# Kernel tuning notes

Hardware: AMD Instinct MI355X
Metric: run time of the kernel (lower is better)

Reference implementation:

```python
import jax, jax.numpy as jnp
import numpy as np

DIM = 768
NUM_HEADS = 12
SCALE = 1.0 / (DIM ** 0.5)  # NOTE: source scales by 1/sqrt(dim), not 1/sqrt(head_dim)


def setup_inputs() -> dict:
    key = jax.random.key(0)
    k_x, k_qkv, k_ow, k_ob = jax.random.split(key, 4)
    b, n = 8, 1024
    x = jax.random.normal(k_x, (b, n, DIM), dtype=jnp.float32)
    # torch Linear weight is [out, in]; we store jax-style [in, out]
    w_qkv = jax.random.normal(k_qkv, (DIM, 3 * DIM), dtype=jnp.float32) * (DIM ** -0.5)
    w_out = jax.random.normal(k_ow, (DIM, DIM), dtype=jnp.float32) * (DIM ** -0.5)
    b_out = jax.random.normal(k_ob, (DIM,), dtype=jnp.float32) * 0.01
    return {"x": x, "w_qkv": w_qkv, "w_out": w_out, "b_out": b_out}


def reference(x, w_qkv, w_out, b_out):
    b, n, c = x.shape
    h = NUM_HEADS
    hd = c // h
    qkv = (x @ w_qkv).reshape(b, n, 3, h, hd)
    q, k, v = jnp.moveaxis(qkv, 2, 0)          # each [b, n, h, hd]
    q = jnp.swapaxes(q, 1, 2)                  # [b, h, n, hd]
    k = jnp.swapaxes(k, 1, 2)
    v = jnp.swapaxes(v, 1, 2)
    dot = jnp.einsum('bhqd,bhkd->bhqk', q, k) * SCALE
    attn = jax.nn.softmax(dot, axis=-1)        # attn_dropout p=0 -> identity
    out = jnp.einsum('bhqk,bhkd->bhqd', attn, v)
    out = jnp.swapaxes(out, 1, 2).reshape(b, n, c)
    return out @ w_out + b_out                 # proj_dropout p=0 -> identity
```

## Files before the change

kernel.cpp:

```cpp
#include <hip/hip_runtime.h>

#define DEV __device__ __forceinline__

typedef __bf16 bf16x8 __attribute__((ext_vector_type(8)));
typedef float  f32x4  __attribute__((ext_vector_type(4)));
typedef float  f32x16 __attribute__((ext_vector_type(16)));
typedef unsigned int u32x4 __attribute__((ext_vector_type(4)));

static constexpr float SCALE = 0.036084391824351615f;
static constexpr float L2E   = 1.4426950408889634f;

DEV unsigned short f2bf(float f) {
  return __builtin_bit_cast(unsigned short, (__bf16)f);
}
DEV unsigned int pack2(float a, float b) {
  return (unsigned int)f2bf(a) | ((unsigned int)f2bf(b) << 16);
}

#define GLDS16(gp, lp) \
  __builtin_amdgcn_global_load_lds((__attribute__((address_space(1))) void*)(gp), \
                                   (__attribute__((address_space(3))) void*)(lp), 16, 0, 0)

__global__ __launch_bounds__(256) void k_prep(const float* __restrict__ x,
                                              const float* __restrict__ w_qkv,
                                              const float* __restrict__ w_out,
                                              unsigned short* __restrict__ xb,
                                              unsigned short* __restrict__ wqkvT,
                                              unsigned short* __restrict__ woutT) {
  __shared__ float tile[64][65];
  int b = blockIdx.x, t = threadIdx.x;
  if (b < 3072) {
    int i = b * 256 + t;
    const float4* p = (const float4*)x + (size_t)i * 2;
    float4 a = p[0], bb = p[1];
    uint4 r;
    r.x = pack2(a.x, a.y); r.y = pack2(a.z, a.w);
    r.z = pack2(bb.x, bb.y); r.w = pack2(bb.z, bb.w);
    ((uint4*)xb)[i] = r;
    return;
  }
  const float* in;
  unsigned short* out;
  int R, C, bx, by;
  if (b < 3504) {
    int tt = b - 3072; in = w_qkv; out = wqkvT; R = 768; C = 2304;
    bx = tt % 36; by = tt / 36;
  } else {
    int tt = b - 3504; in = w_out; out = woutT; R = 768; C = 768;
    bx = tt % 12; by = tt / 12;
  }
  int c0 = bx * 64, r0 = by * 64;
  int tr = t >> 6, tc = t & 63;
#pragma unroll
  for (int i = 0; i < 64; i += 4)
    tile[i + tr][tc] = in[(size_t)(r0 + i + tr) * C + c0 + tc];
  __syncthreads();
#pragma unroll
  for (int i = 0; i < 64; i += 4)
    out[(size_t)(c0 + i + tr) * R + r0 + tc] = f2bf(tile[tc][i + tr]);
}

__global__ __launch_bounds__(512, 4) void k_gemm1(const unsigned short* __restrict__ A,
                                                  const unsigned short* __restrict__ BT,
                                                  unsigned short* __restrict__ Qb,
                                                  unsigned short* __restrict__ Kb,
                                                  unsigned short* __restrict__ VTb) {
  __shared__ __align__(16) char smem[49152];
  char* As = smem;
  char* Bs = smem + 16384;
  const int tid = threadIdx.x;
  const int wave = tid >> 6, lane = tid & 63;
  const int g = lane >> 4, l15 = lane & 15;
  const int wrow = wave >> 2, wcol = wave & 3;

  int id = blockIdx.y * gridDim.x + blockIdx.x;
  int per_xcd = (gridDim.x * gridDim.y) >> 3;
  int id2 = (id & 7) * per_xcd + (id >> 3);
  const int bm = id2 / gridDim.x, bn = id2 % gridDim.x;

  f32x4 acc[4][4] = {};
  const unsigned short* Abase = A + (size_t)bm * 128 * 768;
  const unsigned short* Bbase = BT + (size_t)bn * 256 * 768;

  for (int kt = 0; kt < 12; ++kt) {
    const int k0 = kt * 64;
#pragma unroll
    for (int i = 0; i < 2; ++i) {
      int q = i * 512 + tid;
      int row = q >> 3, c = q & 7;
      int cs = c ^ (row & 7);
      GLDS16(Abase + (size_t)row * 768 + k0 + cs * 8, As + (i * 512 + wave * 64) * 16);
    }
#pragma unroll
    for (int i = 0; i < 4; ++i) {
      int q = i * 512 + tid;
      int row = q >> 3, c = q & 7;
      int cs = c ^ (row & 7);
      GLDS16(Bbase + (size_t)row * 768 + k0 + cs * 8, Bs + (i * 512 + wave * 64) * 16);
    }
    __syncthreads();
    __builtin_amdgcn_s_setprio(1);
#pragma unroll
    for (int kk = 0; kk < 2; ++kk) {
      bf16x8 af[4], bfr[4];
#pragma unroll
      for (int mi = 0; mi < 4; ++mi) {
        int r = wrow * 64 + mi * 16 + l15;
        af[mi] = *(const bf16x8*)(As + r * 128 + (((kk * 4 + g) ^ (r & 7)) * 16));
      }
#pragma unroll
      for (int ni = 0; ni < 4; ++ni) {
        int r = wcol * 64 + ni * 16 + l15;
        bfr[ni] = *(const bf16x8*)(Bs + r * 128 + (((kk * 4 + g) ^ (r & 7)) * 16));
      }
#pragma unroll
      for (int mi = 0; mi < 4; ++mi)
#pragma unroll
        for (int ni = 0; ni < 4; ++ni)
          acc[mi][ni] = __builtin_amdgcn_mfma_f32_16x16x32_bf16(af[mi], bfr[ni], acc[mi][ni], 0, 0, 0);
    }
    __builtin_amdgcn_s_setprio(0);
    __syncthreads();
  }

  const int row0 = bm * 128 + wrow * 64;
  const int col0 = bn * 256 + wcol * 64;
#pragma unroll
  for (int mi = 0; mi < 4; ++mi) {
#pragma unroll
    for (int ni = 0; ni < 4; ++ni) {
      int col = col0 + ni * 16 + l15;
      int which = col / 768;
      int hd = col - which * 768;
      int head = hd >> 6, d = hd & 63;
      int rowm0 = row0 + mi * 16 + g * 4;
      int bi = rowm0 >> 10, np = rowm0 & 1023;
      if (which == 0) {
#pragma unroll
        for (int j = 0; j < 4; ++j)
          Qb[((size_t)(bi * 12 + head) * 1024 + np + j) * 64 + d] =
              f2bf(acc[mi][ni][j] * (SCALE * L2E));
      } else if (which == 1) {
#pragma unroll
        for (int j = 0; j < 4; ++j)
          Kb[((size_t)(bi * 12 + head) * 1024 + np + j) * 64 + d] = f2bf(acc[mi][ni][j]);
      } else {
        ushort4 w;
        w.x = f2bf(acc[mi][ni][0]); w.y = f2bf(acc[mi][ni][1]);
        w.z = f2bf(acc[mi][ni][2]); w.w = f2bf(acc[mi][ni][3]);
        *(ushort4*)(VTb + ((size_t)(bi * 12 + head) * 64 + d) * 1024 + np) = w;
      }
    }
  }
}

__global__ __launch_bounds__(256) void k_gemm2(const unsigned short* __restrict__ A,
                                               const unsigned short* __restrict__ BT,
                                               float* __restrict__ out,
                                               const float* __restrict__ bias) {
  __shared__ __align__(16) char smem[65536];
  const int tid = threadIdx.x;
  const int wave = tid >> 6, lane = tid & 63;
  const int g = lane >> 4, l15 = lane & 15;
  const int wrow = wave >> 1, wcol = wave & 1;

  int id = blockIdx.y * gridDim.x + blockIdx.x;
  int per_xcd = (gridDim.x * gridDim.y) >> 3;
  int id2 = (id & 7) * per_xcd + (id >> 3);
  const int bm = id2 / gridDim.x, bn = id2 % gridDim.x;

  f32x4 acc[4][4] = {};
  const unsigned short* Abase = A + (size_t)bm * 128 * 768;
  const unsigned short* Bbase = BT + (size_t)bn * 128 * 768;

  auto STAGE = [&](int buf, int kt) {
    const int k0 = kt * 64;
#pragma unroll
    for (int i = 0; i < 4; ++i) {
      int q = i * 256 + tid;
      int row = q >> 3, c = q & 7;
      int cs = c ^ (row & 7);
      GLDS16(Abase + (size_t)row * 768 + k0 + cs * 8,
             smem + buf * 32768 + (i * 256 + wave * 64) * 16);
      GLDS16(Bbase + (size_t)row * 768 + k0 + cs * 8,
             smem + buf * 32768 + 16384 + (i * 256 + wave * 64) * 16);
    }
  };

  STAGE(0, 0);
  __syncthreads();

#pragma unroll
  for (int kt = 0; kt < 12; ++kt) {
    const int cur = kt & 1;
    if (kt < 11) STAGE(cur ^ 1, kt + 1);
    char* As = smem + cur * 32768;
    char* Bs = As + 16384;
    __builtin_amdgcn_s_setprio(1);
#pragma unroll
    for (int kk = 0; kk < 2; ++kk) {
      bf16x8 af[4], bfr[4];
#pragma unroll
      for (int mi = 0; mi < 4; ++mi) {
        int r = wrow * 64 + mi * 16 + l15;
        af[mi] = *(const bf16x8*)(As + r * 128 + (((kk * 4 + g) ^ (r & 7)) * 16));
      }
#pragma unroll
      for (int ni = 0; ni < 4; ++ni) {
        int r = wcol * 64 + ni * 16 + l15;
        bfr[ni] = *(const bf16x8*)(Bs + r * 128 + (((kk * 4 + g) ^ (r & 7)) * 16));
      }
#pragma unroll
      for (int mi = 0; mi < 4; ++mi)
#pragma unroll
        for (int ni = 0; ni < 4; ++ni)
          acc[mi][ni] = __builtin_amdgcn_mfma_f32_16x16x32_bf16(af[mi], bfr[ni], acc[mi][ni], 0, 0, 0);
    }
    __builtin_amdgcn_s_setprio(0);
    __syncthreads();
  }

  const int row0 = bm * 128 + wrow * 64;
  const int col0 = bn * 128 + wcol * 64;
#pragma unroll
  for (int mi = 0; mi < 4; ++mi) {
#pragma unroll
    for (int ni = 0; ni < 4; ++ni) {
      int col = col0 + ni * 16 + l15;
      float bz = bias[col];
#pragma unroll
      for (int j = 0; j < 4; ++j) {
        int rowm = row0 + mi * 16 + g * 4 + j;
        out[(size_t)rowm * 768 + col] = acc[mi][ni][j] + bz;
      }
    }
  }
}

__global__ __launch_bounds__(256, 3) void k_attn(const unsigned short* __restrict__ Qb,
                                                 const unsigned short* __restrict__ Kb,
                                                 const unsigned short* __restrict__ VTb,
                                                 unsigned short* __restrict__ Ao) {
  __shared__ __align__(16) char smem[32768];
  const int tid = threadIdx.x, wave = tid >> 6, lane = tid & 63;
  const int hi = lane >> 5, q31 = lane & 31;
  const int bh = blockIdx.x % 96, qt = blockIdx.x / 96;
  const int qbase = qt * 128 + wave * 32;
  const unsigned short* Kp = Kb + (size_t)bh * 65536;
  const unsigned short* Vp = VTb + (size_t)bh * 65536;

  auto STAGE = [&](int buf, int kt) {
#pragma unroll
    for (int i = 0; i < 2; ++i) {
      int c = i * 4 + wave;
      GLDS16(Kp + (size_t)(kt * 64 + lane) * 64 + c * 8,
             smem + buf * 8192 + (i * 256 + wave * 64) * 16);
      GLDS16(Vp + (size_t)lane * 1024 + kt * 64 + c * 8,
             smem + 16384 + buf * 8192 + (i * 256 + wave * 64) * 16);
    }
  };

  bf16x8 aq[4];
#pragma unroll
  for (int dk = 0; dk < 4; ++dk)
    aq[dk] = *(const bf16x8*)(Qb + (size_t)bh * 65536 +
                              (size_t)(qbase + q31) * 64 + dk * 16 + hi * 8);

  bf16x8 vones;
#pragma unroll
  for (int e = 0; e < 8; ++e) vones[e] = (__bf16)1.0f;

  f32x16 o0 = {}, o1 = {};
  f32x16 lacc = {};

  STAGE(0, 0);
  __syncthreads();

#pragma unroll 2
  for (int kt = 0; kt < 16; ++kt) {
    const int cur = kt & 1;
    if (kt < 15) STAGE(cur ^ 1, kt + 1);
    char* Ks = smem + cur * 8192;
    char* Vs = smem + 16384 + cur * 8192;

    f32x16 st0 = {}, st1 = {};
    __builtin_amdgcn_s_setprio(1);
#pragma unroll
    for (int dk = 0; dk < 4; ++dk) {
      bf16x8 ka0 = *(const bf16x8*)(Ks + (((dk * 2 + hi) * 64 + q31) * 16));
      bf16x8 ka1 = *(const bf16x8*)(Ks + (((dk * 2 + hi) * 64 + 32 + q31) * 16));
      st0 = __builtin_amdgcn_mfma_f32_32x32x16_bf16(ka0, aq[dk], st0, 0, 0, 0);
      st1 = __builtin_amdgcn_mfma_f32_32x32x16_bf16(ka1, aq[dk], st1, 0, 0, 0);
    }
    __builtin_amdgcn_s_setprio(0);

#pragma unroll
    for (int sub = 0; sub < 2; ++sub) {
      const f32x16& st = sub ? st1 : st0;
      float ex[16];
#pragma unroll
      for (int r2 = 0; r2 < 16; ++r2) ex[r2] = __builtin_amdgcn_exp2f(st[r2]);

      unsigned w00 = pack2(ex[0], ex[1]),   w01 = pack2(ex[2], ex[3]);
      unsigned w10 = pack2(ex[4], ex[5]),   w11 = pack2(ex[6], ex[7]);
      unsigned w20 = pack2(ex[8], ex[9]),   w21 = pack2(ex[10], ex[11]);
      unsigned w30 = pack2(ex[12], ex[13]), w31 = pack2(ex[14], ex[15]);

      auto pA = __builtin_amdgcn_permlane32_swap(w00, w10, false, false);
      auto pB = __builtin_amdgcn_permlane32_swap(w01, w11, false, false);
      auto pC = __builtin_amdgcn_permlane32_swap(w20, w30, false, false);
      auto pD = __builtin_amdgcn_permlane32_swap(w21, w31, false, false);

      __builtin_amdgcn_s_setprio(1);
#pragma unroll
      for (int s = 0; s < 2; ++s) {
        u32x4 au;
        if (s == 0) { au[0] = pA[0]; au[1] = pB[0]; au[2] = pA[1]; au[3] = pB[1]; }
        else        { au[0] = pC[0]; au[1] = pD[0]; au[2] = pC[1]; au[3] = pD[1]; }
        bf16x8 pa = __builtin_bit_cast(bf16x8, au);
        int ch = sub * 4 + s * 2 + hi;
        bf16x8 vb0 = *(const bf16x8*)(Vs + (ch * 64 + q31) * 16);
        bf16x8 vb1 = *(const bf16x8*)(Vs + (ch * 64 + 32 + q31) * 16);
        o0   = __builtin_amdgcn_mfma_f32_32x32x16_bf16(pa, vb0, o0, 0, 0, 0);
        o1   = __builtin_amdgcn_mfma_f32_32x32x16_bf16(pa, vb1, o1, 0, 0, 0);
        lacc = __builtin_amdgcn_mfma_f32_32x32x16_bf16(pa, vones, lacc, 0, 0, 0);
      }
      __builtin_amdgcn_s_setprio(0);
    }

    __syncthreads();
  }

  const int b_idx = bh / 12, h = bh - b_idx * 12;
#pragma unroll
  for (int m = 0; m < 4; ++m) {
#pragma unroll
    for (int j = 0; j < 4; ++j) {
      int reg = m * 4 + j;
      int qr = j + 8 * m + 4 * hi;
      float linv = 1.0f / lacc[reg];
      size_t base = (size_t)(b_idx * 1024 + qbase + qr) * 768 + h * 64 + q31;
      Ao[base]      = f2bf(o0[reg] * linv);
      Ao[base + 32] = f2bf(o1[reg] * linv);
    }
  }
}


extern "C" void kernel_launch(void* const* d_in, const int* in_sizes, int n_in,
                              void* d_out, int out_size, void* d_ws, size_t ws_size,
                              hipStream_t stream) {
  const float* x     = (const float*)d_in[0];
  const float* w_qkv = (const float*)d_in[1];
  const float* w_out = (const float*)d_in[2];
  const float* b_out = (const float*)d_in[3];

  char* ws = (char*)d_ws;
  size_t off = 0;
  auto alloc = [&](size_t bytes) {
    void* p = ws + off;
    off += (bytes + 255) & ~(size_t)255;
    return p;
  };
  unsigned short* xb    = (unsigned short*)alloc(8192ull * 768 * 2);
  unsigned short* wqkvT = (unsigned short*)alloc(2304ull * 768 * 2);
  unsigned short* woutT = (unsigned short*)alloc(768ull * 768 * 2);
  unsigned short* Qb    = (unsigned short*)alloc(96ull * 1024 * 64 * 2);
  unsigned short* Kbf   = (unsigned short*)alloc(96ull * 1024 * 64 * 2);
  unsigned short* VTb   = (unsigned short*)alloc(96ull * 1024 * 64 * 2);
  unsigned short* Aob   = (unsigned short*)alloc(96ull * 1024 * 64 * 2);

  k_prep<<<3648, 256, 0, stream>>>(x, w_qkv, w_out, xb, wqkvT, woutT);
  k_gemm1<<<dim3(9, 64), 512, 0, stream>>>(xb, wqkvT, Qb, Kbf, VTb);
  k_attn<<<768, 256, 0, stream>>>(Qb, Kbf, VTb, Aob);
  k_gemm2<<<dim3(6, 64), 256, 0, stream>>>(Aob, woutT, (float*)d_out, b_out);
}
```

Baseline: 108.2 us.

## Restructure QKV GEMM into 256x256 tiles with a 9-slot LDS ring pipeline

The QKV projection GEMM moves from 128x256 tiles with a single LDS buffer to 256x256 tiles, launched as 288 blocks with 144KB of dynamic shared memory arranged as a ring of nine 16KB half-tiles. Global-to-LDS loads for the next k-steps are issued between MFMA quarter-phases, with explicit vmcnt and lgkmcnt waits and raw barriers, so memory traffic overlaps compute. The aim is higher operand reuse and hidden load latency. The cost is lower occupancy (2 blocks per CU at most, likely 1 given the LDS size), more registers for the 8x4 accumulators, and a fragile hand-written synchronisation scheme.

```diff
diff --git a/kernel.cpp b/kernel.cpp
--- a/kernel.cpp
+++ b/kernel.cpp
@@ -60,73 +60,157 @@
     out[(size_t)(c0 + i + tr) * R + r0 + tc] = f2bf(tile[tc][i + tr]);
 }
 
-__global__ __launch_bounds__(512, 4) void k_gemm1(const unsigned short* __restrict__ A,
+__global__ __launch_bounds__(512, 2) void k_gemm1(const unsigned short* __restrict__ A,
                                                   const unsigned short* __restrict__ BT,
                                                   unsigned short* __restrict__ Qb,
                                                   unsigned short* __restrict__ Kb,
                                                   unsigned short* __restrict__ VTb) {
-  __shared__ __align__(16) char smem[49152];
-  char* As = smem;
-  char* Bs = smem + 16384;
+  extern __shared__ __align__(16) char smem[];
   const int tid = threadIdx.x;
   const int wave = tid >> 6, lane = tid & 63;
   const int g = lane >> 4, l15 = lane & 15;
-  const int wrow = wave >> 2, wcol = wave & 3;
-
-  int id = blockIdx.y * gridDim.x + blockIdx.x;
-  int per_xcd = (gridDim.x * gridDim.y) >> 3;
-  int id2 = (id & 7) * per_xcd + (id >> 3);
-  const int bm = id2 / gridDim.x, bn = id2 % gridDim.x;
-
-  f32x4 acc[4][4] = {};
-  const unsigned short* Abase = A + (size_t)bm * 128 * 768;
+  const int wr = wave >> 2, wc = wave & 3;
+
+  int id = blockIdx.x;
+  int id2 = (id & 7) * 36 + (id >> 3);
+  const int bm = id2 / 9, bn = id2 % 9;
+
+  const unsigned short* Abase = A + (size_t)bm * 256 * 768;
   const unsigned short* Bbase = BT + (size_t)bn * 256 * 768;
 
-  for (int kt = 0; kt < 12; ++kt) {
-    const int k0 = kt * 64;
+  f32x4 acc[8][4] = {};
+  bf16x8 bfr[4];
+
+  auto STAGE = [&](int slot, int mat, int h, int t) {
+    const unsigned short* src = (mat ? Bbase : Abase) + (size_t)h * 128 * 768 + t * 64;
+    char* dst = smem + slot * 16384;
 #pragma unroll
     for (int i = 0; i < 2; ++i) {
       int q = i * 512 + tid;
       int row = q >> 3, c = q & 7;
       int cs = c ^ (row & 7);
-      GLDS16(Abase + (size_t)row * 768 + k0 + cs * 8, As + (i * 512 + wave * 64) * 16);
-    }
-#pragma unroll
-    for (int i = 0; i < 4; ++i) {
-      int q = i * 512 + tid;
-      int row = q >> 3, c = q & 7;
-      int cs = c ^ (row & 7);
-      GLDS16(Bbase + (size_t)row * 768 + k0 + cs * 8, Bs + (i * 512 + wave * 64) * 16);
-    }
-    __syncthreads();
-    __builtin_amdgcn_s_setprio(1);
-#pragma unroll
-    for (int kk = 0; kk < 2; ++kk) {
-      bf16x8 af[4], bfr[4];
-#pragma unroll
-      for (int mi = 0; mi < 4; ++mi) {
-        int r = wrow * 64 + mi * 16 + l15;
-        af[mi] = *(const bf16x8*)(As + r * 128 + (((kk * 4 + g) ^ (r & 7)) * 16));
-      }
-#pragma unroll
-      for (int ni = 0; ni < 4; ++ni) {
-        int r = wcol * 64 + ni * 16 + l15;
-        bfr[ni] = *(const bf16x8*)(Bs + r * 128 + (((kk * 4 + g) ^ (r & 7)) * 16));
-      }
+      GLDS16(src + (size_t)row * 768 + cs * 8, dst + (i * 512 + wave * 64) * 16);
+    }
+    asm volatile("" ::: "memory");
+  };
+
+  STAGE(0, 0, 0, 0); STAGE(1, 0, 1, 0); STAGE(2, 1, 0, 0); STAGE(3, 1, 1, 0);
+  STAGE(4, 0, 0, 1);
+  asm volatile("s_waitcnt vmcnt(2)" ::: "memory");
+  __builtin_amdgcn_s_barrier();
+
+  int sbase = 0;
+  for (int T = 0; T < 12; ++T) {
+    int sA = sbase + wr;            if (sA >= 9) sA -= 9;
+    int sB = sbase + 2 + (wc >> 1); if (sB >= 9) sB -= 9;
+    const char* Ab = smem + sA * 16384;
+    const char* Bb = smem + sB * 16384;
+    const int rB = (wc & 1) * 64;
+    int ss0 = sbase + 5; if (ss0 >= 9) ss0 -= 9;
+    int ss1 = ss0 + 1;   if (ss1 >= 9) ss1 -= 9;
+    int ss2 = ss1 + 1;   if (ss2 >= 9) ss2 -= 9;
+    int ss3 = ss2 + 1;   if (ss3 >= 9) ss3 -= 9;
+    const bool st1 = (T + 1 < 12), st2 = (T + 2 < 12);
+
+    {
+      bf16x8 af[4];
+#pragma unroll
+      for (int i = 0; i < 4; ++i) {
+        int r = i * 16 + l15;
+        af[i] = *(const bf16x8*)(Ab + r * 128 + ((g ^ (r & 7)) * 16));
+      }
+#pragma unroll
+      for (int i = 0; i < 4; ++i) {
+        int r = rB + i * 16 + l15;
+        bfr[i] = *(const bf16x8*)(Bb + r * 128 + ((g ^ (r & 7)) * 16));
+      }
+      if (st1) STAGE(ss0, 0, 1, T + 1);
+      __builtin_amdgcn_s_barrier();
+      asm volatile("s_waitcnt lgkmcnt(0)" ::: "memory");
+      __builtin_amdgcn_s_setprio(1);
 #pragma unroll
       for (int mi = 0; mi < 4; ++mi)
 #pragma unroll
         for (int ni = 0; ni < 4; ++ni)
           acc[mi][ni] = __builtin_amdgcn_mfma_f32_16x16x32_bf16(af[mi], bfr[ni], acc[mi][ni], 0, 0, 0);
-    }
-    __builtin_amdgcn_s_setprio(0);
-    __syncthreads();
-  }
-
-  const int row0 = bm * 128 + wrow * 64;
-  const int col0 = bn * 256 + wcol * 64;
-#pragma unroll
-  for (int mi = 0; mi < 4; ++mi) {
+      __builtin_amdgcn_s_setprio(0);
+      __builtin_amdgcn_s_barrier();
+    }
+    {
+      bf16x8 af[4];
+#pragma unroll
+      for (int i = 0; i < 4; ++i) {
+        int r = 64 + i * 16 + l15;
+        af[i] = *(const bf16x8*)(Ab + r * 128 + ((g ^ (r & 7)) * 16));
+      }
+      if (st1) STAGE(ss1, 1, 0, T + 1);
+      __builtin_amdgcn_s_barrier();
+      asm volatile("s_waitcnt lgkmcnt(0)" ::: "memory");
+      __builtin_amdgcn_s_setprio(1);
+#pragma unroll
+      for (int mi = 0; mi < 4; ++mi)
+#pragma unroll
+        for (int ni = 0; ni < 4; ++ni)
+          acc[4 + mi][ni] = __builtin_amdgcn_mfma_f32_16x16x32_bf16(af[mi], bfr[ni], acc[4 + mi][ni], 0, 0, 0);
+      __builtin_amdgcn_s_setprio(0);
+      __builtin_amdgcn_s_barrier();
+    }
+    {
+      bf16x8 af[4];
+#pragma unroll
+      for (int i = 0; i < 4; ++i) {
+        int r = i * 16 + l15;
+        af[i] = *(const bf16x8*)(Ab + r * 128 + (((4 + g) ^ (r & 7)) * 16));
+      }
+#pragma unroll
+      for (int i = 0; i < 4; ++i) {
+        int r = rB + i * 16 + l15;
+        bfr[i] = *(const bf16x8*)(Bb + r * 128 + (((4 + g) ^ (r & 7)) * 16));
+      }
+      if (st1) STAGE(ss2, 1, 1, T + 1);
+      __builtin_amdgcn_s_barrier();
+      asm volatile("s_waitcnt lgkmcnt(0)" ::: "memory");
+      __builtin_amdgcn_s_setprio(1);
+#pragma unroll
+      for (int mi = 0; mi < 4; ++mi)
+#pragma unroll
+        for (int ni = 0; ni < 4; ++ni)
+          acc[mi][ni] = __builtin_amdgcn_mfma_f32_16x16x32_bf16(af[mi], bfr[ni], acc[mi][ni], 0, 0, 0);
+      __builtin_amdgcn_s_setprio(0);
+      __builtin_amdgcn_s_barrier();
+    }
+    {
+      bf16x8 af[4];
+#pragma unroll
+      for (int i = 0; i < 4; ++i) {
+        int r = 64 + i * 16 + l15;
+        af[i] = *(const bf16x8*)(Ab + r * 128 + (((4 + g) ^ (r & 7)) * 16));
+      }
+      if (st2) {
+        STAGE(ss3, 0, 0, T + 2);
+        asm volatile("s_waitcnt vmcnt(2)" ::: "memory");
+      } else if (T == 10) {
+        asm volatile("s_waitcnt vmcnt(0)" ::: "memory");
+      }
+      __builtin_amdgcn_s_barrier();
+      asm volatile("s_waitcnt lgkmcnt(0)" ::: "memory");
+      __builtin_amdgcn_s_setprio(1);
+#pragma unroll
+      for (int mi = 0; mi < 4; ++mi)
+#pragma unroll
+        for (int ni = 0; ni < 4; ++ni)
+          acc[4 + mi][ni] = __builtin_amdgcn_mfma_f32_16x16x32_bf16(af[mi], bfr[ni], acc[4 + mi][ni], 0, 0, 0);
+      __builtin_amdgcn_s_setprio(0);
+      __builtin_amdgcn_s_barrier();
+    }
+
+    sbase += 4; if (sbase >= 9) sbase -= 9;
+  }
+
+  const int row0 = bm * 256 + wr * 128;
+  const int col0 = bn * 256 + wc * 64;
+#pragma unroll
+  for (int mi = 0; mi < 8; ++mi) {
 #pragma unroll
     for (int ni = 0; ni < 4; ++ni) {
       int col = col0 + ni * 16 + l15;
@@ -370,8 +454,11 @@
   unsigned short* VTb   = (unsigned short*)alloc(96ull * 1024 * 64 * 2);
   unsigned short* Aob   = (unsigned short*)alloc(96ull * 1024 * 64 * 2);
 
+  hipFuncSetAttribute(reinterpret_cast<const void*>(k_gemm1),
+                      hipFuncAttributeMaxDynamicSharedMemorySize, 147456);
+
   k_prep<<<3648, 256, 0, stream>>>(x, w_qkv, w_out, xb, wqkvT, woutT);
-  k_gemm1<<<dim3(9, 64), 512, 0, stream>>>(xb, wqkvT, Qb, Kbf, VTb);
+  k_gemm1<<<288, 512, 147456, stream>>>(xb, wqkvT, Qb, Kbf, VTb);
   k_attn<<<768, 256, 0, stream>>>(Qb, Kbf, VTb, Aob);
   k_gemm2<<<dim3(6, 64), 256, 0, stream>>>(Aob, woutT, (float*)d_out, b_out);
 }
```

Measured after the change: 115.7 us. 6.9% more time.
